# Kernel optimization log

Hardware: AMD Instinct MI355X
Metric: run time of the kernel (lower is better)

## Reference

```python
import jax, jax.numpy as jnp
import numpy as np


def setup_inputs() -> dict:
    key = jax.random.key(0)
    ks = jax.random.split(key, 20)
    B, T, E, U, D, O = 64, 2048, 256, 256, 256, 32000
    s = lambda k, shp, fan: (jax.random.normal(k, shp, jnp.float32) * (1.0 / np.sqrt(fan)))
    return {
        'inputs': jax.random.normal(ks[0], (B, D), jnp.float32),
        'stm': jax.random.normal(ks[1], (B, U), jnp.float32),
        'x_seq': jax.random.normal(ks[2], (B, T, E), jnp.float32),
        'V_a': s(ks[3], (U + E,), U + E),
        'W_a': s(ks[4], (U + E, U + E), U + E),
        'W_r': s(ks[5], (D, U), D), 'U_r': s(ks[6], (U, U), U), 'C_r': s(ks[7], (E, U), E), 'b_r': jnp.zeros((U,), jnp.float32),
        'W_z': s(ks[8], (D, U), D), 'U_z': s(ks[9], (U, U), U), 'C_z': s(ks[10], (E, U), E), 'b_z': jnp.zeros((U,), jnp.float32),
        'W_p': s(ks[11], (D, U), D), 'U_p': s(ks[12], (U, U), U), 'C_p': s(ks[13], (E, U), E), 'b_p': jnp.zeros((U,), jnp.float32),
        'W_o': s(ks[14], (D, O), D), 'U_o': s(ks[15], (U, O), U), 'C_o': s(ks[16], (E, O), E), 'b_o': jnp.zeros((O,), jnp.float32),
    }


def reference(inputs, stm, x_seq, V_a, W_a,
              W_r, U_r, C_r, b_r,
              W_z, U_z, C_z, b_z,
              W_p, U_p, C_p, b_p,
              W_o, U_o, C_o, b_o):
    B, T, E = x_seq.shape
    U = stm.shape[-1]
    # Bahdanau additive attention: concat repeated state with encoder seq
    _stm = jnp.broadcast_to(stm[:, None, :], (B, T, U))          # [B,T,U]
    cat = jnp.concatenate([_stm, x_seq], axis=-1)                 # [B,T,U+E]
    et = jnp.einsum('btc,c->bt', jnp.tanh(jnp.einsum('btc,cd->btd', cat, W_a)), V_a)
    at = jax.nn.softmax(et, axis=1)                               # exp / sum over T
    context = jnp.einsum('bt,bte->be', at, x_seq)                 # [B,E]
    # GRU-style gates conditioned on input, previous state, and context
    rt = jax.nn.sigmoid(inputs @ W_r + stm @ U_r + context @ C_r + b_r)
    zt = jax.nn.sigmoid(inputs @ W_z + stm @ U_z + context @ C_z + b_z)
    s_tp = jnp.tanh(inputs @ W_p + (rt * stm) @ U_p + context @ C_p + b_p)
    st = (1.0 - zt) * stm + zt * s_tp                             # new state [B,U]
    output = jax.nn.softmax(inputs @ W_o + stm @ U_o + context @ C_o + b_o, axis=-1)  # [B,O]
    return output, st
```

## Files before the change

kernel.cpp:

```cpp
#include <hip/hip_runtime.h>

#define B_ 64
#define T_ 2048
#define E_ 256
#define U_ 256
#define O_ 32000
#define UE_ 512

typedef __attribute__((ext_vector_type(8))) short bf16x8;
typedef __attribute__((ext_vector_type(4))) float f32x4;

__device__ __forceinline__ unsigned short f2bf(float f){
  unsigned u = __builtin_bit_cast(unsigned, f);
  u = u + 0x7FFFu + ((u >> 16) & 1u);
  return (unsigned short)(u >> 16);
}
__device__ __forceinline__ unsigned pk2bf(float a, float b){
  return (unsigned)f2bf(a) | ((unsigned)f2bf(b) << 16);
}
__device__ __forceinline__ bf16x8 pack8(const float* v0, const float* v1){
  float4 x = *(const float4*)v0;
  float4 y = *(const float4*)v1;
  uint4 pk;
  pk.x = pk2bf(x.x, x.y); pk.y = pk2bf(x.z, x.w);
  pk.z = pk2bf(y.x, y.y); pk.w = pk2bf(y.z, y.w);
  return __builtin_bit_cast(bf16x8, pk);
}
__device__ __forceinline__ float ftanh(float x){
  float e = __expf(2.0f*x);
  return 1.0f - 2.0f/(e + 1.0f);
}
__device__ __forceinline__ float fsig(float x){
  return 1.0f/(1.0f + __expf(-x));
}

__global__ void pack_b_kernel(const float* __restrict__ Wa, unsigned short* __restrict__ bpack){
  int idx = blockIdx.x*256 + threadIdx.x;
  int n = idx & 511;
  int ktg = idx >> 9;
  int erow = ktg * 8;
  unsigned short o[8];
#pragma unroll
  for (int i = 0; i < 8; ++i)
    o[i] = f2bf(Wa[(256 + erow + i)*512 + n]);
  uint4 v;
  v.x = (unsigned)o[0] | ((unsigned)o[1] << 16);
  v.y = (unsigned)o[2] | ((unsigned)o[3] << 16);
  v.z = (unsigned)o[4] | ((unsigned)o[5] << 16);
  v.w = (unsigned)o[6] | ((unsigned)o[7] << 16);
  ((uint4*)bpack)[idx] = v;
}

__global__ __launch_bounds__(256)
void stmpart_mfma_kernel(const float* __restrict__ stm, const float* __restrict__ Wa,
                         float* __restrict__ sp){
  int tid = threadIdx.x;
  int w = tid >> 6, l = tid & 63, c = l & 15, g = l >> 4;
  int n0 = blockIdx.x*64 + w*16;
  f32x4 zero = {0.f,0.f,0.f,0.f};
  f32x4 acc[4];
#pragma unroll
  for (int mt = 0; mt < 4; ++mt) acc[mt] = zero;
#pragma unroll
  for (int ks = 0; ks < 8; ++ks){
    int kg = ks*32 + 8*g;
    bf16x8 a[4];
#pragma unroll
    for (int mt = 0; mt < 4; ++mt){
      const float* ap = stm + (mt*16 + c)*256 + kg;
      a[mt] = pack8(ap, ap + 4);
    }
    const float* bp = Wa + (size_t)kg*512 + n0 + c;
    float bv[8];
#pragma unroll
    for (int i = 0; i < 8; ++i) bv[i] = bp[(size_t)i*512];
    uint4 pk;
    pk.x = pk2bf(bv[0], bv[1]); pk.y = pk2bf(bv[2], bv[3]);
    pk.z = pk2bf(bv[4], bv[5]); pk.w = pk2bf(bv[6], bv[7]);
    bf16x8 bfr = __builtin_bit_cast(bf16x8, pk);
#pragma unroll
    for (int mt = 0; mt < 4; ++mt)
      acc[mt] = __builtin_amdgcn_mfma_f32_16x16x32_bf16(a[mt], bfr, acc[mt], 0, 0, 0);
  }
#pragma unroll
  for (int mt = 0; mt < 4; ++mt)
#pragma unroll
    for (int r = 0; r < 4; ++r){
      int m = mt*16 + 4*g + r;
      sp[m*512 + n0 + c] = acc[mt][r];
    }
}

#define LDA 264
__global__ __launch_bounds__(512, 4)
void et_kernel(const float* __restrict__ xseq, const unsigned short* __restrict__ bpack,
               const float* __restrict__ va, const float* __restrict__ sp,
               float* __restrict__ et){
  __shared__ unsigned short sA[64*LDA];
  __shared__ float sVa[512];
  __shared__ float sSp[512];
  __shared__ float sEt[8][64];
  int tid = threadIdx.x;
  int m0 = blockIdx.x * 64;
  int b  = m0 >> 11;

  const float4* x4 = (const float4*)xseq + (size_t)m0 * 64;
#pragma unroll
  for (int i = 0; i < 8; ++i){
    int p = i*512 + tid;
    int row = p >> 6, kq = p & 63;
    float4 v = x4[row*64 + kq];
    uint2 u;
    u.x = pk2bf(v.x, v.y);
    u.y = pk2bf(v.z, v.w);
    *(uint2*)&sA[row*LDA + kq*4] = u;
  }
  sVa[tid < 512 ? tid : 0] = va[tid];
  sSp[tid] = sp[b*512 + tid];
  __syncthreads();

  int w = tid >> 6, l = tid & 63, c = l & 15, g = l >> 4;
  f32x4 zero = {0.f, 0.f, 0.f, 0.f};
  f32x4 acc[4][4];
#pragma unroll
  for (int mt = 0; mt < 4; ++mt)
#pragma unroll
    for (int nt = 0; nt < 4; ++nt) acc[mt][nt] = zero;

  const bf16x8* bp = (const bf16x8*)bpack;
#pragma unroll
  for (int ks = 0; ks < 8; ++ks){
    bf16x8 a[4], bb[4];
#pragma unroll
    for (int mt = 0; mt < 4; ++mt)
      a[mt] = *(const bf16x8*)&sA[(mt*16 + c)*LDA + ks*32 + 8*g];
    int bbase = (ks*4 + g)*512 + w*64 + c;
#pragma unroll
    for (int nt = 0; nt < 4; ++nt)
      bb[nt] = bp[bbase + nt*16];
#pragma unroll
    for (int mt = 0; mt < 4; ++mt)
#pragma unroll
      for (int nt = 0; nt < 4; ++nt)
        acc[mt][nt] = __builtin_amdgcn_mfma_f32_16x16x32_bf16(a[mt], bb[nt], acc[mt][nt], 0, 0, 0);
  }

  float pr[4][4];
#pragma unroll
  for (int mt = 0; mt < 4; ++mt)
#pragma unroll
    for (int r = 0; r < 4; ++r){
      float p = 0.f;
#pragma unroll
      for (int nt = 0; nt < 4; ++nt){
        int n = w*64 + nt*16 + c;
        float v = acc[mt][nt][r] + sSp[n];
        p += sVa[n] * ftanh(v);
      }
      pr[mt][r] = p;
    }
#pragma unroll
  for (int mask = 1; mask < 16; mask <<= 1){
#pragma unroll
    for (int mt = 0; mt < 4; ++mt)
#pragma unroll
      for (int r = 0; r < 4; ++r)
        pr[mt][r] += __shfl_xor(pr[mt][r], mask, 64);
  }
  if (c == 0){
#pragma unroll
    for (int mt = 0; mt < 4; ++mt)
#pragma unroll
      for (int r = 0; r < 4; ++r)
        sEt[w][mt*16 + 4*g + r] = pr[mt][r];
  }
  __syncthreads();
  if (tid < 64){
    float e = 0.f;
#pragma unroll
    for (int ww = 0; ww < 8; ++ww) e += sEt[ww][tid];
    et[m0 + tid] = e;
  }
}

__global__ void at_kernel(const float* __restrict__ et, float* __restrict__ at){
  __shared__ float red[4];
  __shared__ float red2[4];
  int b = blockIdx.x, tid = threadIdx.x;
  float v[8];
#pragma unroll
  for (int i = 0; i < 8; ++i) v[i] = et[b*2048 + i*256 + tid];
  float m = v[0];
#pragma unroll
  for (int i = 1; i < 8; ++i) m = fmaxf(m, v[i]);
#pragma unroll
  for (int off = 1; off < 64; off <<= 1) m = fmaxf(m, __shfl_xor(m, off, 64));
  int wv = tid >> 6;
  if ((tid & 63) == 0) red[wv] = m;
  __syncthreads();
  m = fmaxf(fmaxf(red[0], red[1]), fmaxf(red[2], red[3]));
  float e[8]; float s = 0.f;
#pragma unroll
  for (int i = 0; i < 8; ++i){ e[i] = __expf(v[i] - m); s += e[i]; }
#pragma unroll
  for (int off = 1; off < 64; off <<= 1) s += __shfl_xor(s, off, 64);
  if ((tid & 63) == 0) red2[wv] = s;
  __syncthreads();
  s = red2[0] + red2[1] + red2[2] + red2[3];
  float inv = 1.0f / s;
#pragma unroll
  for (int i = 0; i < 8; ++i) at[b*2048 + i*256 + tid] = e[i] * inv;
}

__global__ void ctxpart_kernel(const float* __restrict__ at, const float* __restrict__ xseq,
                               float* __restrict__ cp){
  __shared__ float s_at[256];
  int ch = blockIdx.x;
  int b  = blockIdx.y;
  int e  = threadIdx.x;
  int t0 = ch * 256;
  s_at[e] = at[b*2048 + t0 + e];
  __syncthreads();
  float acc = 0.f;
  const float* xp = xseq + ((size_t)(b*2048 + t0))*256 + e;
#pragma unroll 4
  for (int tt = 0; tt < 256; ++tt)
    acc += s_at[tt] * xp[(size_t)tt * 256];
  cp[(b*8 + ch)*256 + e] = acc;
}

__global__ void ctx_x1_kernel(const float* __restrict__ cp, const float* __restrict__ inputs,
                              const float* __restrict__ stm,
                              unsigned short* __restrict__ X1bf){
  int b = blockIdx.x, e = threadIdx.x;
  float s = 0.f;
#pragma unroll
  for (int c = 0; c < 8; ++c) s += cp[(b*8 + c)*256 + e];
  X1bf[b*768 + e]        = f2bf(inputs[b*256 + e]);
  X1bf[b*768 + 256 + e]  = f2bf(stm[b*256 + e]);
  X1bf[b*768 + 512 + e]  = f2bf(s);
}

__global__ __launch_bounds__(256)
void gates1_kernel(const unsigned short* __restrict__ X1bf, const float* __restrict__ stm,
                   const float* __restrict__ Wr, const float* __restrict__ Ur,
                   const float* __restrict__ Cr, const float* __restrict__ brr,
                   const float* __restrict__ Wz, const float* __restrict__ Uz,
                   const float* __restrict__ Cz, const float* __restrict__ bzz,
                   const float* __restrict__ Wp, const float* __restrict__ Cp,
                   const float* __restrict__ bpp,
                   float* __restrict__ rs, float* __restrict__ ztb, float* __restrict__ pic){
  int tid = threadIdx.x;
  int w = tid >> 6, l = tid & 63, c = l & 15, g = l >> 4;
  int n0 = blockIdx.x*64 + w*16;
  int gate = n0 >> 8;
  int col0 = n0 & 255;
  const float* W0; const float* W1; const float* W2; const float* bias;
  if (gate == 0){ W0 = Wr; W1 = Ur; W2 = Cr; bias = brr; }
  else if (gate == 1){ W0 = Wz; W1 = Uz; W2 = Cz; bias = bzz; }
  else { W0 = Wp; W1 = nullptr; W2 = Cp; bias = bpp; }

  f32x4 zero = {0.f,0.f,0.f,0.f};
  f32x4 acc[4];
#pragma unroll
  for (int mt = 0; mt < 4; ++mt) acc[mt] = zero;

#pragma unroll
  for (int ph = 0; ph < 3; ++ph){
    const float* src = (ph == 0) ? W0 : (ph == 1) ? W1 : W2;
    if (src == nullptr) continue;
#pragma unroll
    for (int ks = 0; ks < 8; ++ks){
      int kg = ks*32 + 8*g;
      bf16x8 a[4];
#pragma unroll
      for (int mt = 0; mt < 4; ++mt)
        a[mt] = *(const bf16x8*)&X1bf[(mt*16 + c)*768 + ph*256 + kg];
      const float* bp = src + (size_t)kg*256 + col0 + c;
      float bv[8];
#pragma unroll
      for (int i = 0; i < 8; ++i) bv[i] = bp[(size_t)i*256];
      uint4 pk;
      pk.x = pk2bf(bv[0], bv[1]); pk.y = pk2bf(bv[2], bv[3]);
      pk.z = pk2bf(bv[4], bv[5]); pk.w = pk2bf(bv[6], bv[7]);
      bf16x8 bfr = __builtin_bit_cast(bf16x8, pk);
#pragma unroll
      for (int mt = 0; mt < 4; ++mt)
        acc[mt] = __builtin_amdgcn_mfma_f32_16x16x32_bf16(a[mt], bfr, acc[mt], 0, 0, 0);
    }
  }

  int n = col0 + c;
  float bi = bias[n];
#pragma unroll
  for (int mt = 0; mt < 4; ++mt)
#pragma unroll
    for (int r = 0; r < 4; ++r){
      int m = mt*16 + 4*g + r;
      float pre = acc[mt][r] + bi;
      if (gate == 0)      rs[m*256 + n]  = fsig(pre) * stm[m*256 + n];
      else if (gate == 1) ztb[m*256 + n] = fsig(pre);
      else                pic[m*256 + n] = pre;
    }
}

__global__ __launch_bounds__(256)
void gates2_kernel(const float* __restrict__ rs, const float* __restrict__ Up,
                   const float* __restrict__ pic, const float* __restrict__ ztb,
                   const float* __restrict__ stm, float* __restrict__ stout){
  int tid = threadIdx.x;
  int w = tid >> 6, l = tid & 63, c = l & 15, g = l >> 4;
  int n0 = blockIdx.x*64 + w*16;
  f32x4 zero = {0.f,0.f,0.f,0.f};
  f32x4 acc[4];
#pragma unroll
  for (int mt = 0; mt < 4; ++mt) acc[mt] = zero;
#pragma unroll
  for (int ks = 0; ks < 8; ++ks){
    int kg = ks*32 + 8*g;
    bf16x8 a[4];
#pragma unroll
    for (int mt = 0; mt < 4; ++mt){
      const float* ap = rs + (mt*16 + c)*256 + kg;
      a[mt] = pack8(ap, ap + 4);
    }
    const float* bp = Up + (size_t)kg*256 + n0 + c;
    float bv[8];
#pragma unroll
    for (int i = 0; i < 8; ++i) bv[i] = bp[(size_t)i*256];
    uint4 pk;
    pk.x = pk2bf(bv[0], bv[1]); pk.y = pk2bf(bv[2], bv[3]);
    pk.z = pk2bf(bv[4], bv[5]); pk.w = pk2bf(bv[6], bv[7]);
    bf16x8 bfr = __builtin_bit_cast(bf16x8, pk);
#pragma unroll
    for (int mt = 0; mt < 4; ++mt)
      acc[mt] = __builtin_amdgcn_mfma_f32_16x16x32_bf16(a[mt], bfr, acc[mt], 0, 0, 0);
  }
#pragma unroll
  for (int mt = 0; mt < 4; ++mt)
#pragma unroll
    for (int r = 0; r < 4; ++r){
      int m = mt*16 + 4*g + r;
      int o = m*256 + n0 + c;
      float ap = pic[o] + acc[mt][r];
      float z = ztb[o];
      stout[o] = (1.f - z)*stm[o] + z*ftanh(ap);
    }
}

__global__ __launch_bounds__(256)
void logits_mfma_kernel(const unsigned short* __restrict__ X1bf,
                        const float* __restrict__ Wo, const float* __restrict__ Uo,
                        const float* __restrict__ Co, const float* __restrict__ boo,
                        float* __restrict__ outl){
  int tid = threadIdx.x;
  int w = tid >> 6, l = tid & 63, c = l & 15, g = l >> 4;
  int n0 = blockIdx.x*64 + w*16;
  f32x4 zero = {0.f,0.f,0.f,0.f};
  f32x4 acc[4];
#pragma unroll
  for (int mt = 0; mt < 4; ++mt) acc[mt] = zero;

#pragma unroll
  for (int ph = 0; ph < 3; ++ph){
    const float* src = (ph == 0) ? Wo : (ph == 1) ? Uo : Co;
#pragma unroll 2
    for (int ks = 0; ks < 8; ++ks){
      int kg = ph*256 + ks*32 + 8*g;
      bf16x8 a[4];
#pragma unroll
      for (int mt = 0; mt < 4; ++mt)
        a[mt] = *(const bf16x8*)&X1bf[(mt*16 + c)*768 + kg];
      const float* bp = src + (size_t)(ks*32 + 8*g)*32000 + n0 + c;
      float bv[8];
#pragma unroll
      for (int i = 0; i < 8; ++i) bv[i] = bp[(size_t)i*32000];
      uint4 pk;
      pk.x = pk2bf(bv[0], bv[1]);
      pk.y = pk2bf(bv[2], bv[3]);
      pk.z = pk2bf(bv[4], bv[5]);
      pk.w = pk2bf(bv[6], bv[7]);
      bf16x8 bfr = __builtin_bit_cast(bf16x8, pk);
#pragma unroll
      for (int mt = 0; mt < 4; ++mt)
        acc[mt] = __builtin_amdgcn_mfma_f32_16x16x32_bf16(a[mt], bfr, acc[mt], 0, 0, 0);
    }
  }

  float bias = boo[n0 + c];
#pragma unroll
  for (int mt = 0; mt < 4; ++mt)
#pragma unroll
    for (int r = 0; r < 4; ++r){
      int m = mt*16 + 4*g + r;
      outl[(size_t)m*32000 + n0 + c] = acc[mt][r] + bias;
    }
}

__global__ void sm_part_kernel(const float* __restrict__ logits, float* __restrict__ part){
  __shared__ float red[4];
  __shared__ float red2[4];
  int bid = blockIdx.x;
  int b = bid >> 3, ch = bid & 7;
  int base = b*32000 + ch*4000;
  int tid = threadIdx.x;
  float v[16];
#pragma unroll
  for (int i = 0; i < 16; ++i){
    int idx = i*256 + tid;
    v[i] = (idx < 4000) ? logits[base + idx] : -INFINITY;
  }
  float m = v[0];
#pragma unroll
  for (int i = 1; i < 16; ++i) m = fmaxf(m, v[i]);
#pragma unroll
  for (int off = 1; off < 64; off <<= 1) m = fmaxf(m, __shfl_xor(m, off, 64));
  int wv = tid >> 6;
  if ((tid & 63) == 0) red[wv] = m;
  __syncthreads();
  m = fmaxf(fmaxf(red[0], red[1]), fmaxf(red[2], red[3]));
  float s = 0.f;
#pragma unroll
  for (int i = 0; i < 16; ++i) s += __expf(v[i] - m);
#pragma unroll
  for (int off = 1; off < 64; off <<= 1) s += __shfl_xor(s, off, 64);
  if ((tid & 63) == 0) red2[wv] = s;
  __syncthreads();
  if (tid == 0){
    float st = red2[0] + red2[1] + red2[2] + red2[3];
    part[bid*2]     = m;
    part[bid*2 + 1] = st;
  }
}

__global__ void sm_comb_kernel(const float* __restrict__ part, float* __restrict__ fin){
  int b = threadIdx.x;
  float M = -INFINITY;
#pragma unroll
  for (int c = 0; c < 8; ++c) M = fmaxf(M, part[(b*8 + c)*2]);
  float S = 0.f;
#pragma unroll
  for (int c = 0; c < 8; ++c) S += part[(b*8 + c)*2 + 1] * __expf(part[(b*8 + c)*2] - M);
  fin[2*b] = M;
  fin[2*b + 1] = S;
}

__global__ void sm_norm_kernel(float* __restrict__ logits, const float* __restrict__ fin){
  int bid = blockIdx.x;
  int b = bid >> 3, ch = bid & 7;
  int base = b*32000 + ch*4000;
  int tid = threadIdx.x;
  float M = fin[2*b];
  float inv = 1.0f / fin[2*b + 1];
#pragma unroll
  for (int i = 0; i < 16; ++i){
    int idx = i*256 + tid;
    if (idx < 4000){
      int o = base + idx;
      logits[o] = __expf(logits[o] - M) * inv;
    }
  }
}

extern "C" void kernel_launch(void* const* d_in, const int* in_sizes, int n_in,
                              void* d_out, int out_size, void* d_ws, size_t ws_size,
                              hipStream_t stream) {
  const float* inputs = (const float*)d_in[0];
  const float* stm    = (const float*)d_in[1];
  const float* xseq   = (const float*)d_in[2];
  const float* Va     = (const float*)d_in[3];
  const float* Wa     = (const float*)d_in[4];
  const float* Wr = (const float*)d_in[5];
  const float* Ur = (const float*)d_in[6];
  const float* Cr = (const float*)d_in[7];
  const float* br = (const float*)d_in[8];
  const float* Wz = (const float*)d_in[9];
  const float* Uz = (const float*)d_in[10];
  const float* Cz = (const float*)d_in[11];
  const float* bz = (const float*)d_in[12];
  const float* Wp = (const float*)d_in[13];
  const float* Up = (const float*)d_in[14];
  const float* Cp = (const float*)d_in[15];
  const float* bp = (const float*)d_in[16];
  const float* Wo = (const float*)d_in[17];
  const float* Uo = (const float*)d_in[18];
  const float* Co = (const float*)d_in[19];
  const float* bo = (const float*)d_in[20];

  float* out   = (float*)d_out;
  float* stout = out + (size_t)B_*O_;

  float* wsf = (float*)d_ws;
  unsigned short* bpack = (unsigned short*)d_ws;
  float* sp   = wsf + 65536;
  float* et   = wsf + 98304;
  float* at   = wsf + 229376;
  float* cp   = wsf + 360448;
  unsigned short* X1bf = (unsigned short*)(wsf + 491520);
  float* part = wsf + 516096;
  float* fin  = wsf + 517120;
  float* rs   = wsf + 518144;
  float* ztb  = wsf + 534528;
  float* pic  = wsf + 550912;

  pack_b_kernel<<<64, 256, 0, stream>>>(Wa, bpack);
  stmpart_mfma_kernel<<<8, 256, 0, stream>>>(stm, Wa, sp);
  et_kernel<<<2048, 512, 0, stream>>>(xseq, bpack, Va, sp, et);
  at_kernel<<<64, 256, 0, stream>>>(et, at);
  ctxpart_kernel<<<dim3(8, 64), 256, 0, stream>>>(at, xseq, cp);
  ctx_x1_kernel<<<64, 256, 0, stream>>>(cp, inputs, stm, X1bf);
  gates1_kernel<<<12, 256, 0, stream>>>(X1bf, stm, Wr, Ur, Cr, br,
                                        Wz, Uz, Cz, bz, Wp, Cp, bp,
                                        rs, ztb, pic);
  gates2_kernel<<<4, 256, 0, stream>>>(rs, Up, pic, ztb, stm, stout);
  logits_mfma_kernel<<<500, 256, 0, stream>>>(X1bf, Wo, Uo, Co, bo, out);
  sm_part_kernel<<<512, 256, 0, stream>>>(out, part);
  sm_comb_kernel<<<1, 64, 0, stream>>>(part, fin);
  sm_norm_kernel<<<512, 256, 0, stream>>>(out, fin);
}
```

Baseline: 178.2 us.

## Restructure attention score kernel into persistent 128-row tiles with prefetch

```diff
diff --git a/kernel.cpp b/kernel.cpp
--- a/kernel.cpp
+++ b/kernel.cpp
@@ -6,6 +6,7 @@
 #define U_ 256
 #define O_ 32000
 #define UE_ 512
+#define MROWS 131072
 
 typedef __attribute__((ext_vector_type(8))) short bf16x8;
 typedef __attribute__((ext_vector_type(4))) float f32x4;
@@ -70,10 +71,10 @@
       const float* ap = stm + (mt*16 + c)*256 + kg;
       a[mt] = pack8(ap, ap + 4);
     }
-    const float* bp = Wa + (size_t)kg*512 + n0 + c;
+    const float* bpt = Wa + (size_t)kg*512 + n0 + c;
     float bv[8];
 #pragma unroll
-    for (int i = 0; i < 8; ++i) bv[i] = bp[(size_t)i*512];
+    for (int i = 0; i < 8; ++i) bv[i] = bpt[(size_t)i*512];
     uint4 pk;
     pk.x = pk2bf(bv[0], bv[1]); pk.y = pk2bf(bv[2], bv[3]);
     pk.z = pk2bf(bv[4], bv[5]); pk.w = pk2bf(bv[6], bv[7]);
@@ -91,105 +92,122 @@
     }
 }
 
-#define LDA 264
-__global__ __launch_bounds__(512, 4)
-void et_kernel(const float* __restrict__ xseq, const unsigned short* __restrict__ bpack,
-               const float* __restrict__ va, const float* __restrict__ sp,
-               float* __restrict__ et){
-  __shared__ unsigned short sA[64*LDA];
-  __shared__ float sVa[512];
-  __shared__ float sSp[512];
-  __shared__ float sEt[8][64];
-  int tid = threadIdx.x;
-  int m0 = blockIdx.x * 64;
-  int b  = m0 >> 11;
-
-  const float4* x4 = (const float4*)xseq + (size_t)m0 * 64;
-#pragma unroll
-  for (int i = 0; i < 8; ++i){
-    int p = i*512 + tid;
-    int row = p >> 6, kq = p & 63;
-    float4 v = x4[row*64 + kq];
-    uint2 u;
-    u.x = pk2bf(v.x, v.y);
-    u.y = pk2bf(v.z, v.w);
-    *(uint2*)&sA[row*LDA + kq*4] = u;
-  }
-  sVa[tid < 512 ? tid : 0] = va[tid];
-  sSp[tid] = sp[b*512 + tid];
-  __syncthreads();
-
+__global__ __launch_bounds__(512, 2)
+void et2_kernel(const float* __restrict__ xseq, const unsigned short* __restrict__ bpack,
+                const float* __restrict__ va, const float* __restrict__ sp,
+                float* __restrict__ etp){
+  __shared__ __align__(16) unsigned short sA[32768];
+  uint4* sA4 = (uint4*)sA;
+  int tid = threadIdx.x;
   int w = tid >> 6, l = tid & 63, c = l & 15, g = l >> 4;
-  f32x4 zero = {0.f, 0.f, 0.f, 0.f};
-  f32x4 acc[4][4];
-#pragma unroll
-  for (int mt = 0; mt < 4; ++mt)
-#pragma unroll
-    for (int nt = 0; nt < 4; ++nt) acc[mt][nt] = zero;
-
+  int b = blockIdx.x >> 2;
+
+  float va_r[4], sp_r[4];
+#pragma unroll
+  for (int nt = 0; nt < 4; ++nt){
+    int n = w*64 + nt*16 + c;
+    va_r[nt] = va[n];
+    sp_r[nt] = sp[b*512 + n];
+  }
+
+  int r = tid & 127, jb = tid >> 7;
+  int mt_w = r >> 4, cr = r & 15;
+  const float4* x4 = (const float4*)xseq;
   const bf16x8* bp = (const bf16x8*)bpack;
-#pragma unroll
-  for (int ks = 0; ks < 8; ++ks){
-    bf16x8 a[4], bb[4];
-#pragma unroll
-    for (int mt = 0; mt < 4; ++mt)
-      a[mt] = *(const bf16x8*)&sA[(mt*16 + c)*LDA + ks*32 + 8*g];
-    int bbase = (ks*4 + g)*512 + w*64 + c;
-#pragma unroll
-    for (int nt = 0; nt < 4; ++nt)
-      bb[nt] = bp[bbase + nt*16];
-#pragma unroll
-    for (int mt = 0; mt < 4; ++mt)
-#pragma unroll
-      for (int nt = 0; nt < 4; ++nt)
-        acc[mt][nt] = __builtin_amdgcn_mfma_f32_16x16x32_bf16(a[mt], bb[nt], acc[mt][nt], 0, 0, 0);
-  }
-
-  float pr[4][4];
-#pragma unroll
-  for (int mt = 0; mt < 4; ++mt)
-#pragma unroll
-    for (int r = 0; r < 4; ++r){
-      float p = 0.f;
-#pragma unroll
-      for (int nt = 0; nt < 4; ++nt){
-        int n = w*64 + nt*16 + c;
-        float v = acc[mt][nt][r] + sSp[n];
-        p += sVa[n] * ftanh(v);
+
+  float4 f[8];
+  {
+    size_t fb = ((size_t)(blockIdx.x*512 + r))*64 + 2*jb;
+#pragma unroll
+    for (int i = 0; i < 4; ++i){ f[2*i] = x4[fb + 8*i]; f[2*i+1] = x4[fb + 8*i + 1]; }
+  }
+
+  for (int t = 0; t < 4; ++t){
+    int m0 = blockIdx.x*512 + t*128;
+
+#pragma unroll
+    for (int i = 0; i < 4; ++i){
+      uint4 pk;
+      pk.x = pk2bf(f[2*i].x,   f[2*i].y);   pk.y = pk2bf(f[2*i].z,   f[2*i].w);
+      pk.z = pk2bf(f[2*i+1].x, f[2*i+1].y); pk.w = pk2bf(f[2*i+1].z, f[2*i+1].w);
+      sA4[(mt_w*8 + i)*64 + jb*16 + cr] = pk;
+    }
+    {
+      size_t fb2 = ((size_t)(m0 + r))*64 + 32 + 2*jb;
+#pragma unroll
+      for (int i = 0; i < 4; ++i){ f[2*i] = x4[fb2 + 8*i]; f[2*i+1] = x4[fb2 + 8*i + 1]; }
+#pragma unroll
+      for (int i = 0; i < 4; ++i){
+        uint4 pk;
+        pk.x = pk2bf(f[2*i].x,   f[2*i].y);   pk.y = pk2bf(f[2*i].z,   f[2*i].w);
+        pk.z = pk2bf(f[2*i+1].x, f[2*i+1].y); pk.w = pk2bf(f[2*i+1].z, f[2*i+1].w);
+        sA4[(mt_w*8 + 4 + i)*64 + jb*16 + cr] = pk;
       }
-      pr[mt][r] = p;
-    }
-#pragma unroll
-  for (int mask = 1; mask < 16; mask <<= 1){
-#pragma unroll
-    for (int mt = 0; mt < 4; ++mt)
-#pragma unroll
-      for (int r = 0; r < 4; ++r)
-        pr[mt][r] += __shfl_xor(pr[mt][r], mask, 64);
-  }
-  if (c == 0){
-#pragma unroll
-    for (int mt = 0; mt < 4; ++mt)
-#pragma unroll
-      for (int r = 0; r < 4; ++r)
-        sEt[w][mt*16 + 4*g + r] = pr[mt][r];
-  }
-  __syncthreads();
-  if (tid < 64){
-    float e = 0.f;
-#pragma unroll
-    for (int ww = 0; ww < 8; ++ww) e += sEt[ww][tid];
-    et[m0 + tid] = e;
-  }
-}
-
-__global__ void at_kernel(const float* __restrict__ et, float* __restrict__ at){
+    }
+    __syncthreads();
+
+    if (t < 3){
+      size_t fbn = ((size_t)(m0 + 128 + r))*64 + 2*jb;
+#pragma unroll
+      for (int i = 0; i < 4; ++i){ f[2*i] = x4[fbn + 8*i]; f[2*i+1] = x4[fbn + 8*i + 1]; }
+    }
+
+    f32x4 zero = {0.f,0.f,0.f,0.f};
+    f32x4 acc[8][4];
+#pragma unroll
+    for (int mt = 0; mt < 8; ++mt)
+#pragma unroll
+      for (int nt = 0; nt < 4; ++nt) acc[mt][nt] = zero;
+
+#pragma unroll
+    for (int ks = 0; ks < 8; ++ks){
+      bf16x8 a[8];
+#pragma unroll
+      for (int mt = 0; mt < 8; ++mt)
+        a[mt] = *(const bf16x8*)&sA4[(mt*8 + ks)*64 + g*16 + c];
+      bf16x8 bb[4];
+      int bbase = (ks*4 + g)*512 + w*64 + c;
+#pragma unroll
+      for (int nt = 0; nt < 4; ++nt) bb[nt] = bp[bbase + nt*16];
+#pragma unroll
+      for (int mt = 0; mt < 8; ++mt)
+#pragma unroll
+        for (int nt = 0; nt < 4; ++nt)
+          acc[mt][nt] = __builtin_amdgcn_mfma_f32_16x16x32_bf16(a[mt], bb[nt], acc[mt][nt], 0, 0, 0);
+    }
+
+#pragma unroll
+    for (int mt = 0; mt < 8; ++mt){
+#pragma unroll
+      for (int r4 = 0; r4 < 4; ++r4){
+        float p = 0.f;
+#pragma unroll
+        for (int nt = 0; nt < 4; ++nt)
+          p += va_r[nt] * ftanh(acc[mt][nt][r4] + sp_r[nt]);
+#pragma unroll
+        for (int mask = 1; mask < 16; mask <<= 1)
+          p += __shfl_xor(p, mask, 64);
+        if (c == 0)
+          etp[w*MROWS + m0 + mt*16 + 4*g + r4] = p;
+      }
+    }
+    __syncthreads();
+  }
+}
+
+__global__ void at_kernel(const float* __restrict__ etp, float* __restrict__ at){
   __shared__ float red[4];
   __shared__ float red2[4];
   int b = blockIdx.x, tid = threadIdx.x;
   float v[8];
 #pragma unroll
-  for (int i = 0; i < 8; ++i) v[i] = et[b*2048 + i*256 + tid];
+  for (int i = 0; i < 8; ++i){
+    float s0 = 0.f;
+#pragma unroll
+    for (int ww = 0; ww < 8; ++ww)
+      s0 += etp[ww*MROWS + b*2048 + i*256 + tid];
+    v[i] = s0;
+  }
   float m = v[0];
 #pragma unroll
   for (int i = 1; i < 8; ++i) m = fmaxf(m, v[i]);
@@ -276,10 +294,10 @@
 #pragma unroll
       for (int mt = 0; mt < 4; ++mt)
         a[mt] = *(const bf16x8*)&X1bf[(mt*16 + c)*768 + ph*256 + kg];
-      const float* bp = src + (size_t)kg*256 + col0 + c;
+      const float* bpt = src + (size_t)kg*256 + col0 + c;
       float bv[8];
 #pragma unroll
-      for (int i = 0; i < 8; ++i) bv[i] = bp[(size_t)i*256];
+      for (int i = 0; i < 8; ++i) bv[i] = bpt[(size_t)i*256];
       uint4 pk;
       pk.x = pk2bf(bv[0], bv[1]); pk.y = pk2bf(bv[2], bv[3]);
       pk.z = pk2bf(bv[4], bv[5]); pk.w = pk2bf(bv[6], bv[7]);
@@ -324,10 +342,10 @@
       const float* ap = rs + (mt*16 + c)*256 + kg;
       a[mt] = pack8(ap, ap + 4);
     }
-    const float* bp = Up + (size_t)kg*256 + n0 + c;
+    const float* bpt = Up + (size_t)kg*256 + n0 + c;
     float bv[8];
 #pragma unroll
-    for (int i = 0; i < 8; ++i) bv[i] = bp[(size_t)i*256];
+    for (int i = 0; i < 8; ++i) bv[i] = bpt[(size_t)i*256];
     uint4 pk;
     pk.x = pk2bf(bv[0], bv[1]); pk.y = pk2bf(bv[2], bv[3]);
     pk.z = pk2bf(bv[4], bv[5]); pk.w = pk2bf(bv[6], bv[7]);
@@ -371,10 +389,10 @@
 #pragma unroll
       for (int mt = 0; mt < 4; ++mt)
         a[mt] = *(const bf16x8*)&X1bf[(mt*16 + c)*768 + kg];
-      const float* bp = src + (size_t)(ks*32 + 8*g)*32000 + n0 + c;
+      const float* bpt = src + (size_t)(ks*32 + 8*g)*32000 + n0 + c;
       float bv[8];
 #pragma unroll
-      for (int i = 0; i < 8; ++i) bv[i] = bp[(size_t)i*32000];
+      for (int i = 0; i < 8; ++i) bv[i] = bpt[(size_t)i*32000];
       uint4 pk;
       pk.x = pk2bf(bv[0], bv[1]);
       pk.y = pk2bf(bv[2], bv[3]);
@@ -493,20 +511,20 @@
   float* wsf = (float*)d_ws;
   unsigned short* bpack = (unsigned short*)d_ws;
   float* sp   = wsf + 65536;
-  float* et   = wsf + 98304;
-  float* at   = wsf + 229376;
-  float* cp   = wsf + 360448;
-  unsigned short* X1bf = (unsigned short*)(wsf + 491520);
-  float* part = wsf + 516096;
-  float* fin  = wsf + 517120;
-  float* rs   = wsf + 518144;
-  float* ztb  = wsf + 534528;
-  float* pic  = wsf + 550912;
+  float* etp  = wsf + 98304;
+  float* at   = wsf + 1146880;
+  float* cp   = wsf + 1277952;
+  unsigned short* X1bf = (unsigned short*)(wsf + 1409024);
+  float* part = wsf + 1433600;
+  float* fin  = wsf + 1434624;
+  float* rs   = wsf + 1434752;
+  float* ztb  = wsf + 1451136;
+  float* pic  = wsf + 1467520;
 
   pack_b_kernel<<<64, 256, 0, stream>>>(Wa, bpack);
   stmpart_mfma_kernel<<<8, 256, 0, stream>>>(stm, Wa, sp);
-  et_kernel<<<2048, 512, 0, stream>>>(xseq, bpack, Va, sp, et);
-  at_kernel<<<64, 256, 0, stream>>>(et, at);
+  et2_kernel<<<256, 512, 0, stream>>>(xseq, bpack, Va, sp, etp);
+  at_kernel<<<64, 256, 0, stream>>>(etp, at);
   ctxpart_kernel<<<dim3(8, 64), 256, 0, stream>>>(at, xseq, cp);
   ctx_x1_kernel<<<64, 256, 0, stream>>>(cp, inputs, stm, X1bf);
   gates1_kernel<<<12, 256, 0, stream>>>(X1bf, stm, Wr, Ur, Cr, br,
```

Result: slower. 263.2 us (+47.6%).

## Double-tile et kernel with register prefetch and swizzled LDS, fuse softmax combine

Applied to the files above, without the earlier changes.

```diff
diff --git a/kernel.cpp b/kernel.cpp
--- a/kernel.cpp
+++ b/kernel.cpp
@@ -70,10 +70,10 @@
       const float* ap = stm + (mt*16 + c)*256 + kg;
       a[mt] = pack8(ap, ap + 4);
     }
-    const float* bp = Wa + (size_t)kg*512 + n0 + c;
+    const float* bpt = Wa + (size_t)kg*512 + n0 + c;
     float bv[8];
 #pragma unroll
-    for (int i = 0; i < 8; ++i) bv[i] = bp[(size_t)i*512];
+    for (int i = 0; i < 8; ++i) bv[i] = bpt[(size_t)i*512];
     uint4 pk;
     pk.x = pk2bf(bv[0], bv[1]); pk.y = pk2bf(bv[2], bv[3]);
     pk.z = pk2bf(bv[4], bv[5]); pk.w = pk2bf(bv[6], bv[7]);
@@ -91,95 +91,113 @@
     }
 }
 
-#define LDA 264
-__global__ __launch_bounds__(512, 4)
-void et_kernel(const float* __restrict__ xseq, const unsigned short* __restrict__ bpack,
-               const float* __restrict__ va, const float* __restrict__ sp,
-               float* __restrict__ et){
-  __shared__ unsigned short sA[64*LDA];
-  __shared__ float sVa[512];
-  __shared__ float sSp[512];
+__global__ __launch_bounds__(512, 3)
+void et3_kernel(const float* __restrict__ xseq, const unsigned short* __restrict__ bpack,
+                const float* __restrict__ va, const float* __restrict__ sp,
+                float* __restrict__ et){
+  __shared__ __align__(16) uint4 sA4[2048];
   __shared__ float sEt[8][64];
   int tid = threadIdx.x;
-  int m0 = blockIdx.x * 64;
-  int b  = m0 >> 11;
-
-  const float4* x4 = (const float4*)xseq + (size_t)m0 * 64;
-#pragma unroll
-  for (int i = 0; i < 8; ++i){
-    int p = i*512 + tid;
-    int row = p >> 6, kq = p & 63;
-    float4 v = x4[row*64 + kq];
-    uint2 u;
-    u.x = pk2bf(v.x, v.y);
-    u.y = pk2bf(v.z, v.w);
-    *(uint2*)&sA[row*LDA + kq*4] = u;
-  }
-  sVa[tid < 512 ? tid : 0] = va[tid];
-  sSp[tid] = sp[b*512 + tid];
-  __syncthreads();
-
   int w = tid >> 6, l = tid & 63, c = l & 15, g = l >> 4;
-  f32x4 zero = {0.f, 0.f, 0.f, 0.f};
-  f32x4 acc[4][4];
-#pragma unroll
-  for (int mt = 0; mt < 4; ++mt)
-#pragma unroll
-    for (int nt = 0; nt < 4; ++nt) acc[mt][nt] = zero;
-
+  int b = blockIdx.x >> 4;
+
+  float va_r[4], sp_r[4];
+#pragma unroll
+  for (int nt = 0; nt < 4; ++nt){
+    int n = w*64 + nt*16 + c;
+    va_r[nt] = va[n];
+    sp_r[nt] = sp[b*512 + n];
+  }
+
+  int r = tid >> 3, jb = tid & 7;
+  const float4* x4 = (const float4*)xseq;
   const bf16x8* bp = (const bf16x8*)bpack;
-#pragma unroll
-  for (int ks = 0; ks < 8; ++ks){
-    bf16x8 a[4], bb[4];
+
+  float4 f[8];
+  {
+    size_t fb = ((size_t)(blockIdx.x*128 + r))*64 + jb*2;
+#pragma unroll
+    for (int i = 0; i < 4; ++i){ f[2*i] = x4[fb + 16*i]; f[2*i+1] = x4[fb + 16*i + 1]; }
+  }
+
+  for (int t = 0; t < 2; ++t){
+    int m0 = blockIdx.x*128 + t*64;
+
+#pragma unroll
+    for (int i = 0; i < 4; ++i){
+      int j = jb + 8*i;
+      int s = ((r>>4)*8 + (j>>2))*64 + (j&3)*16 + (r&15);
+      uint4 pk;
+      pk.x = pk2bf(f[2*i].x,   f[2*i].y);   pk.y = pk2bf(f[2*i].z,   f[2*i].w);
+      pk.z = pk2bf(f[2*i+1].x, f[2*i+1].y); pk.w = pk2bf(f[2*i+1].z, f[2*i+1].w);
+      sA4[s ^ ((s>>4)&7)] = pk;
+    }
+    __syncthreads();
+
+    if (t == 0){
+      size_t fb = ((size_t)(m0 + 64 + r))*64 + jb*2;
+#pragma unroll
+      for (int i = 0; i < 4; ++i){ f[2*i] = x4[fb + 16*i]; f[2*i+1] = x4[fb + 16*i + 1]; }
+    }
+
+    f32x4 zero = {0.f,0.f,0.f,0.f};
+    f32x4 acc[4][4];
 #pragma unroll
     for (int mt = 0; mt < 4; ++mt)
-      a[mt] = *(const bf16x8*)&sA[(mt*16 + c)*LDA + ks*32 + 8*g];
-    int bbase = (ks*4 + g)*512 + w*64 + c;
-#pragma unroll
-    for (int nt = 0; nt < 4; ++nt)
-      bb[nt] = bp[bbase + nt*16];
+#pragma unroll
+      for (int nt = 0; nt < 4; ++nt) acc[mt][nt] = zero;
+
+#pragma unroll
+    for (int ks = 0; ks < 8; ++ks){
+      bf16x8 a[4], bb[4];
+#pragma unroll
+      for (int mt = 0; mt < 4; ++mt){
+        int idx = (mt*8 + ks)*64 + l;
+        a[mt] = *(const bf16x8*)&sA4[idx ^ ((idx>>4)&7)];
+      }
+      int bbase = (ks*4 + g)*512 + w*64 + c;
+#pragma unroll
+      for (int nt = 0; nt < 4; ++nt) bb[nt] = bp[bbase + nt*16];
+#pragma unroll
+      for (int mt = 0; mt < 4; ++mt)
+#pragma unroll
+        for (int nt = 0; nt < 4; ++nt)
+          acc[mt][nt] = __builtin_amdgcn_mfma_f32_16x16x32_bf16(a[mt], bb[nt], acc[mt][nt], 0, 0, 0);
+    }
+
+    float pr[4][4];
 #pragma unroll
     for (int mt = 0; mt < 4; ++mt)
 #pragma unroll
-      for (int nt = 0; nt < 4; ++nt)
-        acc[mt][nt] = __builtin_amdgcn_mfma_f32_16x16x32_bf16(a[mt], bb[nt], acc[mt][nt], 0, 0, 0);
-  }
-
-  float pr[4][4];
-#pragma unroll
-  for (int mt = 0; mt < 4; ++mt)
-#pragma unroll
-    for (int r = 0; r < 4; ++r){
-      float p = 0.f;
-#pragma unroll
-      for (int nt = 0; nt < 4; ++nt){
-        int n = w*64 + nt*16 + c;
-        float v = acc[mt][nt][r] + sSp[n];
-        p += sVa[n] * ftanh(v);
+      for (int r4 = 0; r4 < 4; ++r4){
+        float p = 0.f;
+#pragma unroll
+        for (int nt = 0; nt < 4; ++nt)
+          p += va_r[nt] * ftanh(acc[mt][nt][r4] + sp_r[nt]);
+        pr[mt][r4] = p;
       }
-      pr[mt][r] = p;
-    }
-#pragma unroll
-  for (int mask = 1; mask < 16; mask <<= 1){
-#pragma unroll
-    for (int mt = 0; mt < 4; ++mt)
-#pragma unroll
-      for (int r = 0; r < 4; ++r)
-        pr[mt][r] += __shfl_xor(pr[mt][r], mask, 64);
-  }
-  if (c == 0){
-#pragma unroll
-    for (int mt = 0; mt < 4; ++mt)
-#pragma unroll
-      for (int r = 0; r < 4; ++r)
-        sEt[w][mt*16 + 4*g + r] = pr[mt][r];
-  }
-  __syncthreads();
-  if (tid < 64){
-    float e = 0.f;
-#pragma unroll
-    for (int ww = 0; ww < 8; ++ww) e += sEt[ww][tid];
-    et[m0 + tid] = e;
+#pragma unroll
+    for (int mask = 1; mask < 16; mask <<= 1){
+#pragma unroll
+      for (int mt = 0; mt < 4; ++mt)
+#pragma unroll
+        for (int r4 = 0; r4 < 4; ++r4)
+          pr[mt][r4] += __shfl_xor(pr[mt][r4], mask, 64);
+    }
+    if (c == 0){
+#pragma unroll
+      for (int mt = 0; mt < 4; ++mt)
+#pragma unroll
+        for (int r4 = 0; r4 < 4; ++r4)
+          sEt[w][mt*16 + 4*g + r4] = pr[mt][r4];
+    }
+    __syncthreads();
+    if (tid < 64){
+      float e = 0.f;
+#pragma unroll
+      for (int ww = 0; ww < 8; ++ww) e += sEt[ww][tid];
+      et[m0 + tid] = e;
+    }
   }
 }
 
@@ -276,10 +294,10 @@
 #pragma unroll
       for (int mt = 0; mt < 4; ++mt)
         a[mt] = *(const bf16x8*)&X1bf[(mt*16 + c)*768 + ph*256 + kg];
-      const float* bp = src + (size_t)kg*256 + col0 + c;
+      const float* bpt = src + (size_t)kg*256 + col0 + c;
       float bv[8];
 #pragma unroll
-      for (int i = 0; i < 8; ++i) bv[i] = bp[(size_t)i*256];
+      for (int i = 0; i < 8; ++i) bv[i] = bpt[(size_t)i*256];
       uint4 pk;
       pk.x = pk2bf(bv[0], bv[1]); pk.y = pk2bf(bv[2], bv[3]);
       pk.z = pk2bf(bv[4], bv[5]); pk.w = pk2bf(bv[6], bv[7]);
@@ -324,10 +342,10 @@
       const float* ap = rs + (mt*16 + c)*256 + kg;
       a[mt] = pack8(ap, ap + 4);
     }
-    const float* bp = Up + (size_t)kg*256 + n0 + c;
+    const float* bpt = Up + (size_t)kg*256 + n0 + c;
     float bv[8];
 #pragma unroll
-    for (int i = 0; i < 8; ++i) bv[i] = bp[(size_t)i*256];
+    for (int i = 0; i < 8; ++i) bv[i] = bpt[(size_t)i*256];
     uint4 pk;
     pk.x = pk2bf(bv[0], bv[1]); pk.y = pk2bf(bv[2], bv[3]);
     pk.z = pk2bf(bv[4], bv[5]); pk.w = pk2bf(bv[6], bv[7]);
@@ -371,10 +389,10 @@
 #pragma unroll
       for (int mt = 0; mt < 4; ++mt)
         a[mt] = *(const bf16x8*)&X1bf[(mt*16 + c)*768 + kg];
-      const float* bp = src + (size_t)(ks*32 + 8*g)*32000 + n0 + c;
+      const float* bpt = src + (size_t)(ks*32 + 8*g)*32000 + n0 + c;
       float bv[8];
 #pragma unroll
-      for (int i = 0; i < 8; ++i) bv[i] = bp[(size_t)i*32000];
+      for (int i = 0; i < 8; ++i) bv[i] = bpt[(size_t)i*32000];
       uint4 pk;
       pk.x = pk2bf(bv[0], bv[1]);
       pk.y = pk2bf(bv[2], bv[3]);
@@ -433,25 +451,18 @@
   }
 }
 
-__global__ void sm_comb_kernel(const float* __restrict__ part, float* __restrict__ fin){
-  int b = threadIdx.x;
-  float M = -INFINITY;
-#pragma unroll
-  for (int c = 0; c < 8; ++c) M = fmaxf(M, part[(b*8 + c)*2]);
-  float S = 0.f;
-#pragma unroll
-  for (int c = 0; c < 8; ++c) S += part[(b*8 + c)*2 + 1] * __expf(part[(b*8 + c)*2] - M);
-  fin[2*b] = M;
-  fin[2*b + 1] = S;
-}
-
-__global__ void sm_norm_kernel(float* __restrict__ logits, const float* __restrict__ fin){
+__global__ void sm_norm_kernel(float* __restrict__ logits, const float* __restrict__ part){
   int bid = blockIdx.x;
   int b = bid >> 3, ch = bid & 7;
   int base = b*32000 + ch*4000;
   int tid = threadIdx.x;
-  float M = fin[2*b];
-  float inv = 1.0f / fin[2*b + 1];
+  float M = -INFINITY;
+#pragma unroll
+  for (int cc = 0; cc < 8; ++cc) M = fmaxf(M, part[(b*8 + cc)*2]);
+  float S = 0.f;
+#pragma unroll
+  for (int cc = 0; cc < 8; ++cc) S += part[(b*8 + cc)*2 + 1] * __expf(part[(b*8 + cc)*2] - M);
+  float inv = 1.0f / S;
 #pragma unroll
   for (int i = 0; i < 16; ++i){
     int idx = i*256 + tid;
@@ -498,14 +509,13 @@
   float* cp   = wsf + 360448;
   unsigned short* X1bf = (unsigned short*)(wsf + 491520);
   float* part = wsf + 516096;
-  float* fin  = wsf + 517120;
-  float* rs   = wsf + 518144;
-  float* ztb  = wsf + 534528;
-  float* pic  = wsf + 550912;
+  float* rs   = wsf + 517120;
+  float* ztb  = wsf + 533504;
+  float* pic  = wsf + 549888;
 
   pack_b_kernel<<<64, 256, 0, stream>>>(Wa, bpack);
   stmpart_mfma_kernel<<<8, 256, 0, stream>>>(stm, Wa, sp);
-  et_kernel<<<2048, 512, 0, stream>>>(xseq, bpack, Va, sp, et);
+  et3_kernel<<<1024, 512, 0, stream>>>(xseq, bpack, Va, sp, et);
   at_kernel<<<64, 256, 0, stream>>>(et, at);
   ctxpart_kernel<<<dim3(8, 64), 256, 0, stream>>>(at, xseq, cp);
   ctx_x1_kernel<<<64, 256, 0, stream>>>(cp, inputs, stm, X1bf);
@@ -515,6 +525,5 @@
   gates2_kernel<<<4, 256, 0, stream>>>(rs, Up, pic, ztb, stm, stout);
   logits_mfma_kernel<<<500, 256, 0, stream>>>(X1bf, Wo, Uo, Co, bo, out);
   sm_part_kernel<<<512, 256, 0, stream>>>(out, part);
-  sm_comb_kernel<<<1, 64, 0, stream>>>(part, fin);
-  sm_norm_kernel<<<512, 256, 0, stream>>>(out, fin);
-}
+  sm_norm_kernel<<<512, 256, 0, stream>>>(out, part);
+}
```

Result: slower. 370.5 us (+107.9%).

## Swizzle et_kernel shared A tile, fuse softmax combine into normalize, use hip bf16 conversion

Applied to the files above, without the earlier changes.

```diff
diff --git a/kernel.cpp b/kernel.cpp
--- a/kernel.cpp
+++ b/kernel.cpp
@@ -1,4 +1,5 @@
 #include <hip/hip_runtime.h>
+#include <hip/hip_bf16.h>
 
 #define B_ 64
 #define T_ 2048
@@ -11,9 +12,8 @@
 typedef __attribute__((ext_vector_type(4))) float f32x4;
 
 __device__ __forceinline__ unsigned short f2bf(float f){
-  unsigned u = __builtin_bit_cast(unsigned, f);
-  u = u + 0x7FFFu + ((u >> 16) & 1u);
-  return (unsigned short)(u >> 16);
+  __hip_bfloat16 h = __float2bfloat16(f);
+  return __builtin_bit_cast(unsigned short, h);
 }
 __device__ __forceinline__ unsigned pk2bf(float a, float b){
   return (unsigned)f2bf(a) | ((unsigned)f2bf(b) << 16);
@@ -70,10 +70,10 @@
       const float* ap = stm + (mt*16 + c)*256 + kg;
       a[mt] = pack8(ap, ap + 4);
     }
-    const float* bp = Wa + (size_t)kg*512 + n0 + c;
+    const float* bpt = Wa + (size_t)kg*512 + n0 + c;
     float bv[8];
 #pragma unroll
-    for (int i = 0; i < 8; ++i) bv[i] = bp[(size_t)i*512];
+    for (int i = 0; i < 8; ++i) bv[i] = bpt[(size_t)i*512];
     uint4 pk;
     pk.x = pk2bf(bv[0], bv[1]); pk.y = pk2bf(bv[2], bv[3]);
     pk.z = pk2bf(bv[4], bv[5]); pk.w = pk2bf(bv[6], bv[7]);
@@ -91,12 +91,11 @@
     }
 }
 
-#define LDA 264
 __global__ __launch_bounds__(512, 4)
 void et_kernel(const float* __restrict__ xseq, const unsigned short* __restrict__ bpack,
                const float* __restrict__ va, const float* __restrict__ sp,
                float* __restrict__ et){
-  __shared__ unsigned short sA[64*LDA];
+  __shared__ __align__(16) uint4 sA4[2048];
   __shared__ float sVa[512];
   __shared__ float sSp[512];
   __shared__ float sEt[8][64];
@@ -105,6 +104,7 @@
   int b  = m0 >> 11;
 
   const float4* x4 = (const float4*)xseq + (size_t)m0 * 64;
+  uint2* sA2 = (uint2*)sA4;
 #pragma unroll
   for (int i = 0; i < 8; ++i){
     int p = i*512 + tid;
@@ -113,7 +113,8 @@
     uint2 u;
     u.x = pk2bf(v.x, v.y);
     u.y = pk2bf(v.z, v.w);
-    *(uint2*)&sA[row*LDA + kq*4] = u;
+    int s = ((row>>4)*8 + (kq>>3))*64 + ((kq>>1)&3)*16 + (row&15);
+    sA2[(s ^ ((s>>4)&7))*2 + (kq&1)] = u;
   }
   sVa[tid < 512 ? tid : 0] = va[tid];
   sSp[tid] = sp[b*512 + tid];
@@ -132,8 +133,10 @@
   for (int ks = 0; ks < 8; ++ks){
     bf16x8 a[4], bb[4];
 #pragma unroll
-    for (int mt = 0; mt < 4; ++mt)
-      a[mt] = *(const bf16x8*)&sA[(mt*16 + c)*LDA + ks*32 + 8*g];
+    for (int mt = 0; mt < 4; ++mt){
+      int idx = (mt*8 + ks)*64 + l;
+      a[mt] = *(const bf16x8*)&sA4[idx ^ ((idx>>4)&7)];
+    }
     int bbase = (ks*4 + g)*512 + w*64 + c;
 #pragma unroll
     for (int nt = 0; nt < 4; ++nt)
@@ -276,10 +279,10 @@
 #pragma unroll
       for (int mt = 0; mt < 4; ++mt)
         a[mt] = *(const bf16x8*)&X1bf[(mt*16 + c)*768 + ph*256 + kg];
-      const float* bp = src + (size_t)kg*256 + col0 + c;
+      const float* bpt = src + (size_t)kg*256 + col0 + c;
       float bv[8];
 #pragma unroll
-      for (int i = 0; i < 8; ++i) bv[i] = bp[(size_t)i*256];
+      for (int i = 0; i < 8; ++i) bv[i] = bpt[(size_t)i*256];
       uint4 pk;
       pk.x = pk2bf(bv[0], bv[1]); pk.y = pk2bf(bv[2], bv[3]);
       pk.z = pk2bf(bv[4], bv[5]); pk.w = pk2bf(bv[6], bv[7]);
@@ -324,10 +327,10 @@
       const float* ap = rs + (mt*16 + c)*256 + kg;
       a[mt] = pack8(ap, ap + 4);
     }
-    const float* bp = Up + (size_t)kg*256 + n0 + c;
+    const float* bpt = Up + (size_t)kg*256 + n0 + c;
     float bv[8];
 #pragma unroll
-    for (int i = 0; i < 8; ++i) bv[i] = bp[(size_t)i*256];
+    for (int i = 0; i < 8; ++i) bv[i] = bpt[(size_t)i*256];
     uint4 pk;
     pk.x = pk2bf(bv[0], bv[1]); pk.y = pk2bf(bv[2], bv[3]);
     pk.z = pk2bf(bv[4], bv[5]); pk.w = pk2bf(bv[6], bv[7]);
@@ -371,10 +374,10 @@
 #pragma unroll
       for (int mt = 0; mt < 4; ++mt)
         a[mt] = *(const bf16x8*)&X1bf[(mt*16 + c)*768 + kg];
-      const float* bp = src + (size_t)(ks*32 + 8*g)*32000 + n0 + c;
+      const float* bpt = src + (size_t)(ks*32 + 8*g)*32000 + n0 + c;
       float bv[8];
 #pragma unroll
-      for (int i = 0; i < 8; ++i) bv[i] = bp[(size_t)i*32000];
+      for (int i = 0; i < 8; ++i) bv[i] = bpt[(size_t)i*32000];
       uint4 pk;
       pk.x = pk2bf(bv[0], bv[1]);
       pk.y = pk2bf(bv[2], bv[3]);
@@ -433,25 +436,18 @@
   }
 }
 
-__global__ void sm_comb_kernel(const float* __restrict__ part, float* __restrict__ fin){
-  int b = threadIdx.x;
-  float M = -INFINITY;
-#pragma unroll
-  for (int c = 0; c < 8; ++c) M = fmaxf(M, part[(b*8 + c)*2]);
-  float S = 0.f;
-#pragma unroll
-  for (int c = 0; c < 8; ++c) S += part[(b*8 + c)*2 + 1] * __expf(part[(b*8 + c)*2] - M);
-  fin[2*b] = M;
-  fin[2*b + 1] = S;
-}
-
-__global__ void sm_norm_kernel(float* __restrict__ logits, const float* __restrict__ fin){
+__global__ void sm_norm_kernel(float* __restrict__ logits, const float* __restrict__ part){
   int bid = blockIdx.x;
   int b = bid >> 3, ch = bid & 7;
   int base = b*32000 + ch*4000;
   int tid = threadIdx.x;
-  float M = fin[2*b];
-  float inv = 1.0f / fin[2*b + 1];
+  float M = -INFINITY;
+#pragma unroll
+  for (int cc = 0; cc < 8; ++cc) M = fmaxf(M, part[(b*8 + cc)*2]);
+  float S = 0.f;
+#pragma unroll
+  for (int cc = 0; cc < 8; ++cc) S += part[(b*8 + cc)*2 + 1] * __expf(part[(b*8 + cc)*2] - M);
+  float inv = 1.0f / S;
 #pragma unroll
   for (int i = 0; i < 16; ++i){
     int idx = i*256 + tid;
@@ -498,10 +494,9 @@
   float* cp   = wsf + 360448;
   unsigned short* X1bf = (unsigned short*)(wsf + 491520);
   float* part = wsf + 516096;
-  float* fin  = wsf + 517120;
-  float* rs   = wsf + 518144;
-  float* ztb  = wsf + 534528;
-  float* pic  = wsf + 550912;
+  float* rs   = wsf + 517120;
+  float* ztb  = wsf + 533504;
+  float* pic  = wsf + 549888;
 
   pack_b_kernel<<<64, 256, 0, stream>>>(Wa, bpack);
   stmpart_mfma_kernel<<<8, 256, 0, stream>>>(stm, Wa, sp);
@@ -515,6 +510,5 @@
   gates2_kernel<<<4, 256, 0, stream>>>(rs, Up, pic, ztb, stm, stout);
   logits_mfma_kernel<<<500, 256, 0, stream>>>(X1bf, Wo, Uo, Co, bo, out);
   sm_part_kernel<<<512, 256, 0, stream>>>(out, part);
-  sm_comb_kernel<<<1, 64, 0, stream>>>(part, fin);
-  sm_norm_kernel<<<512, 256, 0, stream>>>(out, fin);
-}
+  sm_norm_kernel<<<512, 256, 0, stream>>>(out, part);
+}
```

After: 175.2 us. No clear change (-1.7%).
